# Optimization experiments

Measured on AMD Instinct MI355X. Metric: run time of the kernel, lower is better.

Reference implementation:

```python
import jax, jax.numpy as jnp
import numpy as np

SMOOTH = 1e-3
N_BASES = 256


def _bases():
    # bases[i, k] = k-th bit (LSB-first) of i, matching f'{i:08b}'[::-1]
    i = np.arange(N_BASES)[:, None]
    k = np.arange(8)[None, :]
    return jnp.asarray(((i >> k) & 1).astype(np.float32))  # [256, 8]


def _unfold(x):
    # x: [B, 2, Y, X] -> [B, 8, (Y+1)*(X+1)], matching F.unfold(kernel=(2,2), padding=1)
    B, C, Y, X = x.shape
    p = jnp.pad(x, ((0, 0), (0, 0), (1, 1), (1, 1)))
    cols = [p[:, c, ky:ky + Y + 1, kx:kx + X + 1]
            for c in range(2) for ky in range(2) for kx in range(2)]
    return jnp.stack(cols, axis=1).reshape(B, 8, (Y + 1) * (X + 1))


def _pair(pred_s, labels, raw, area, bases):
    # pred_s/labels/raw: [B, 2, Y, X]
    up = _unfold(pred_s)                       # [B, 8, L] sigmoid probs
    ul = _unfold(labels)                       # [B, 8, L] float 0/1
    ur = _unfold(raw)                          # [B, 8, L] logits
    uli = ul.astype(jnp.int32)
    B, _, L = up.shape

    # 8-bit neighbour code per point
    label_byte = sum(uli[:, k, :] << k for k in range(8))  # [B, L] int32

    # pred weight of the basis matching each point's label code (gather form of the masked loop)
    sel = bases[label_byte]                    # [B, L, 8]
    w_lab = 1.0 - jnp.linalg.norm(up.transpose(0, 2, 1) - sel, axis=-1) / 16.0  # [B, L]

    # sequential 256-way byte update, faithful to the original python loop
    up_sg = jax.lax.stop_gradient(up)
    d2 = ((up_sg ** 2).sum(1)[:, None, :]
          - 2.0 * jnp.einsum('bkl,nk->bnl', up_sg, bases)
          + (bases ** 2).sum(1)[None, :, None])              # [B, 256, L]
    w_all = 1.0 - jnp.sqrt(jnp.maximum(d2, 0.0)) / 16.0      # [B, 256, L]

    def body(i, byte):
        w = w_all[:, i, :]
        return jnp.where(w > byte.astype(w.dtype), jnp.full_like(byte, 0) + i, byte)

    pred_byte = jax.lax.fori_loop(0, N_BASES, body, jnp.zeros((B, L), jnp.int32))

    pred_areas = area[pred_byte]               # [B, L]
    label_areas = area[label_byte]             # [B, L]
    num = 2.0 * (w_lab * label_areas).sum(1)   # [B]
    denom = label_areas.sum(1) + pred_areas.sum(1)

    # per-batch BCE-with-logits on points whose label cube is empty or full
    mask = ((label_byte == 0) | (label_byte == 255)).astype(up.dtype)  # [B, L]
    x, y = ur, ul
    bce = jnp.maximum(x, 0.0) - x * y + jnp.log1p(jnp.exp(-jnp.abs(x)))  # [B, 8, L]
    vol = (bce * mask[:, None, :]).sum((1, 2)) / (8.0 * mask.sum(1))     # [B]
    return num, denom, vol


def _forward(pred, labels, area):
    pred_s = jax.nn.sigmoid(pred)
    bases = _bases()
    # overlapping z-pairs: [B, Z-1, 2, Y, X] -> vmap over pair axis
    ps = jnp.stack((pred_s[:, :-1], pred_s[:, 1:]), axis=2)
    ls = jnp.stack((labels[:, :-1], labels[:, 1:]), axis=2)
    rs = jnp.stack((pred[:, :-1], pred[:, 1:]), axis=2)
    num, denom, vol = jax.vmap(lambda a, b, c: _pair(a, b, c, area, bases),
                               in_axes=1)(ps, ls, rs)
    num, denom, vol = num.sum(0), denom.sum(0), vol.sum(0)  # [B]
    dice = 1.0 - (num + SMOOTH) / (denom + SMOOTH)
    return dice.mean() + vol.mean()


def setup_inputs() -> dict:
    key = jax.random.key(0)
    k1, k2, k3 = jax.random.split(key, 3)
    pred = jax.random.normal(k1, (2, 12, 192, 192), dtype=jnp.float32)
    labels = jax.random.bernoulli(k2, 0.5, (2, 12, 192, 192)).astype(jnp.float32)
    area = jax.random.uniform(k3, (256,), dtype=jnp.float32) * 2.0
    return {"pred": pred, "labels": labels, "area": area}


def reference(pred, labels, area):
    return _forward(pred, labels, area)
```

## Files before the change

### kernel.cpp

```cpp
#include <hip/hip_runtime.h>
#include <math.h>

#define NYX 192
#define NNODE 193
#define L_NODES (NNODE*NNODE)
#define NPAIR 11
#define NB 2
#define NCH 12
#define NZ 3
#define NGRP (NZ*NB)
#define NBLK 49
#define RECF 12
#define LN2f 0.69314718055994530942f


__global__ __launch_bounds__(256) void sdice_node(const float* __restrict__ pred,
                                                  const float* __restrict__ labels,
                                                  const float* __restrict__ area,
                                                  float* __restrict__ partials)
{
    const int z    = blockIdx.z;
    const int b    = blockIdx.y;
    const int lane = threadIdx.x & 63;
    const int wrow = threadIdx.x >> 6;
    const int j    = blockIdx.x * 4 + wrow;
    const int t    = lane;
    const int np   = (z == 2) ? 3 : 4;
    const int nch  = np + 1;
    const int c0   = z * 4;

    __shared__ float areas[256];
    __shared__ float sred[4][10];
    areas[threadIdx.x] = area[threadIdx.x];
    __syncthreads();

    float numA = 0.f, denA = 0.f;
    float bceA[4] = {0.f, 0.f, 0.f, 0.f};
    float cntA[4] = {0.f, 0.f, 0.f, 0.f};

    const bool act = (j < NNODE) && (t < 48);

    if (act) {
        const int  y0 = (j >= 1) ? (j - 1) : 0;
        const int  y1 = (j <= NYX - 1) ? j : (NYX - 1);
        const int  xo = t * 4;

        float    sigP[2][6], bcvP[2][6], sigC[2][6], bcvC[2][6];
        unsigned w5P[2], w5C[2];

        for (int cc = 0; cc < nch; ++cc) {
            const int ch = c0 + cc;
            const size_t base = (size_t)(b * NCH + ch) * (NYX * NYX);

            #pragma unroll
            for (int r = 0; r < 2; ++r) {
                const int  yy = r ? y1 : y0;
                const bool mm = r ? (j <= NYX - 1) : (j >= 1);
                const float4 p4 = *reinterpret_cast<const float4*>(pred   + base + (size_t)yy * NYX + xo);
                const float4 l4 = *reinterpret_cast<const float4*>(labels + base + (size_t)yy * NYX + xo);
                const float pe[4] = {p4.x, p4.y, p4.z, p4.w};
                const float le[4] = {l4.x, l4.y, l4.z, l4.w};
                unsigned bits = 0;
                #pragma unroll
                for (int e = 0; e < 4; ++e) {
                    const float pv = mm ? pe[e] : 0.f;
                    const float lv = mm ? le[e] : 0.f;
                    bits |= ((unsigned)lv) << e;
                    const float s = __builtin_amdgcn_rcpf(1.f + __expf(-pv));
                    sigC[r][e + 1] = mm ? s : 0.f;
                    bcvC[r][e + 1] = fmaxf(pv, 0.f) - pv * lv + __logf(1.f + __expf(-fabsf(pv)));
                }
                w5C[r] = bits << 1;
                sigC[r][5] = 0.f;
                bcvC[r][5] = LN2f;

                const float    sw = __shfl_up(sigC[r][4], 1);
                const float    bw = __shfl_up(bcvC[r][4], 1);
                const unsigned ww = (unsigned)__shfl_up((int)w5C[r], 1);
                sigC[r][0] = (t == 0) ? 0.f  : sw;
                bcvC[r][0] = (t == 0) ? LN2f : bw;
                w5C[r]    |= (t == 0) ? 0u   : ((ww >> 4) & 1u);
            }

            if (cc > 0) {
                const int pp = cc - 1;
                float pnum = 0.f, pden = 0.f, pbce = 0.f, pcnt = 0.f;
                #pragma unroll
                for (int i = 0; i < 5; ++i) {
                    if (i < 4 || t == 47) {
                        const unsigned b0 = (w5P[0] >> i) & 1u, b1 = (w5P[0] >> (i + 1)) & 1u;
                        const unsigned b2 = (w5P[1] >> i) & 1u, b3 = (w5P[1] >> (i + 1)) & 1u;
                        const unsigned b4 = (w5C[0] >> i) & 1u, b5 = (w5C[0] >> (i + 1)) & 1u;
                        const unsigned b6 = (w5C[1] >> i) & 1u, b7 = (w5C[1] >> (i + 1)) & 1u;
                        const unsigned byte = b0 | (b1 << 1) | (b2 << 2) | (b3 << 3)
                                            | (b4 << 4) | (b5 << 5) | (b6 << 6) | (b7 << 7);
                        float d2 = 0.f;
                        {
                            const float e0 = sigP[0][i]     - (float)b0;
                            const float e1 = sigP[0][i + 1] - (float)b1;
                            const float e2 = sigP[1][i]     - (float)b2;
                            const float e3 = sigP[1][i + 1] - (float)b3;
                            const float e4 = sigC[0][i]     - (float)b4;
                            const float e5 = sigC[0][i + 1] - (float)b5;
                            const float e6 = sigC[1][i]     - (float)b6;
                            const float e7 = sigC[1][i + 1] - (float)b7;
                            d2 = ((e0*e0 + e1*e1) + (e2*e2 + e3*e3)) + ((e4*e4 + e5*e5) + (e6*e6 + e7*e7));
                        }
                        const float w  = 1.f - sqrtf(d2) * (1.f / 16.f);
                        const float la = areas[byte];
                        pnum += w * la;
                        pden += la;
                        const bool msk = (byte == 0u) || (byte == 255u);
                        if (msk) {
                            pcnt += 1.f;
                            pbce += ((bcvP[0][i] + bcvP[0][i+1]) + (bcvP[1][i] + bcvP[1][i+1]))
                                  + ((bcvC[0][i] + bcvC[0][i+1]) + (bcvC[1][i] + bcvC[1][i+1]));
                        }
                    }
                }
                numA += pnum; denA += pden;
                bceA[pp] += pbce; cntA[pp] += pcnt;
            }

            #pragma unroll
            for (int r = 0; r < 2; ++r) {
                w5P[r] = w5C[r];
                #pragma unroll
                for (int q = 0; q < 6; ++q) { sigP[r][q] = sigC[r][q]; bcvP[r][q] = bcvC[r][q]; }
            }
        }
    }


    float v[10] = {numA, denA, bceA[0], bceA[1], bceA[2], bceA[3], cntA[0], cntA[1], cntA[2], cntA[3]};
    #pragma unroll
    for (int off = 32; off > 0; off >>= 1) {
        #pragma unroll
        for (int q = 0; q < 10; ++q) v[q] += __shfl_down(v[q], off);
    }
    if (lane == 0) {
        #pragma unroll
        for (int q = 0; q < 10; ++q) sred[wrow][q] = v[q];
    }
    __syncthreads();
    if (threadIdx.x == 0) {
        float s[10];
        #pragma unroll
        for (int q = 0; q < 10; ++q)
            s[q] = ((sred[0][q] + sred[1][q]) + (sred[2][q] + sred[3][q]));
        float* rec = partials + (size_t)((z * NB + b) * NBLK + blockIdx.x) * RECF;
        #pragma unroll
        for (int q = 0; q < 10; ++q) rec[q] = s[q];
        rec[10] = 0.f; rec[11] = 0.f;
    }
}

__global__ __launch_bounds__(384) void sdice_final(const float* __restrict__ partials,
                                                   const float* __restrict__ area,
                                                   float* __restrict__ out)
{
    __shared__ float gs[NGRP][10];
    const int g    = threadIdx.x >> 6;
    const int lane = threadIdx.x & 63;

    float v[10];
    #pragma unroll
    for (int q = 0; q < 10; ++q) v[q] = 0.f;
    if (lane < NBLK) {
        const float* rec = partials + (size_t)(g * NBLK + lane) * RECF;
        #pragma unroll
        for (int q = 0; q < 10; ++q) v[q] = rec[q];
    }
    #pragma unroll
    for (int off = 32; off > 0; off >>= 1) {
        #pragma unroll
        for (int q = 0; q < 10; ++q) v[q] += __shfl_down(v[q], off);
    }
    if (lane == 0) {
        #pragma unroll
        for (int q = 0; q < 10; ++q) gs[g][q] = v[q];
    }
    __syncthreads();

    if (threadIdx.x == 0) {
        const float a1 = area[1];
        float dice_sum = 0.f, vol_sum = 0.f;
        for (int b = 0; b < NB; ++b) {
            float numb = 0.f, denb = 0.f, volb = 0.f;
            for (int z = 0; z < NZ; ++z) {
                const int g2 = z * NB + b;
                const int np = (z == 2) ? 3 : 4;
                numb += 2.0f * gs[g2][0];
                denb += gs[g2][1];
                for (int pp = 0; pp < np; ++pp)
                    volb += gs[g2][2 + pp] / (8.0f * gs[g2][6 + pp]);
            }
            denb += (float)NPAIR * (float)L_NODES * a1;
            dice_sum += 1.0f - (numb + 0.001f) / (denb + 0.001f);
            vol_sum  += volb;
        }
        out[0] = dice_sum / (float)NB + vol_sum / (float)NB;
    }
}

extern "C" void kernel_launch(void* const* d_in, const int* in_sizes, int n_in,
                              void* d_out, int out_size, void* d_ws, size_t ws_size,
                              hipStream_t stream) {
    const float* pred   = (const float*)d_in[0];
    const float* labels = (const float*)d_in[1];
    const float* area   = (const float*)d_in[2];
    float* out  = (float*)d_out;
    float* part = (float*)d_ws;

    dim3 grid(NBLK, NB, NZ);
    sdice_node<<<grid, dim3(256), 0, stream>>>(pred, labels, area, part);
    sdice_final<<<1, 384, 0, stream>>>(part, area, out);
}
```

Measured before the change: 19.23 us.

## Fuse final reduction into node kernel via atomics and last-block ticket

```diff
diff --git a/kernel.cpp b/kernel.cpp
--- a/kernel.cpp
+++ b/kernel.cpp
@@ -10,14 +10,19 @@
 #define NZ 3
 #define NGRP (NZ*NB)
 #define NBLK 49
-#define RECF 12
+#define NBUCK 4
+#define TOTAL_BLOCKS (NBLK*NB*NZ)
 #define LN2f 0.69314718055994530942f
 
-
-__global__ __launch_bounds__(256) void sdice_node(const float* __restrict__ pred,
-                                                  const float* __restrict__ labels,
-                                                  const float* __restrict__ area,
-                                                  float* __restrict__ partials)
+#define ACC_LINES (NGRP*NBUCK)
+#define TICKET_OFF (ACC_LINES*16*sizeof(float))
+
+__global__ __launch_bounds__(256) void sdice_fused(const float* __restrict__ pred,
+                                                   const float* __restrict__ labels,
+                                                   const float* __restrict__ area,
+                                                   float* __restrict__ acc,
+                                                   unsigned* __restrict__ ticket,
+                                                   float* __restrict__ out)
 {
     const int z    = blockIdx.z;
     const int b    = blockIdx.y;
@@ -31,6 +36,9 @@
 
     __shared__ float areas[256];
     __shared__ float sred[4][10];
+    __shared__ float abuf[NGRP][NBUCK][10];
+    __shared__ float gs[NGRP][10];
+    __shared__ int   lastFlag;
     areas[threadIdx.x] = area[threadIdx.x];
     __syncthreads();
 
@@ -131,7 +139,6 @@
         }
     }
 
-
     float v[10] = {numA, denA, bceA[0], bceA[1], bceA[2], bceA[3], cntA[0], cntA[1], cntA[2], cntA[3]};
     #pragma unroll
     for (int off = 32; off > 0; off >>= 1) {
@@ -143,63 +150,55 @@
         for (int q = 0; q < 10; ++q) sred[wrow][q] = v[q];
     }
     __syncthreads();
+
     if (threadIdx.x == 0) {
         float s[10];
         #pragma unroll
         for (int q = 0; q < 10; ++q)
             s[q] = ((sred[0][q] + sred[1][q]) + (sred[2][q] + sred[3][q]));
-        float* rec = partials + (size_t)((z * NB + b) * NBLK + blockIdx.x) * RECF;
-        #pragma unroll
-        for (int q = 0; q < 10; ++q) rec[q] = s[q];
-        rec[10] = 0.f; rec[11] = 0.f;
-    }
-}
-
-__global__ __launch_bounds__(384) void sdice_final(const float* __restrict__ partials,
-                                                   const float* __restrict__ area,
-                                                   float* __restrict__ out)
-{
-    __shared__ float gs[NGRP][10];
-    const int g    = threadIdx.x >> 6;
-    const int lane = threadIdx.x & 63;
-
-    float v[10];
-    #pragma unroll
-    for (int q = 0; q < 10; ++q) v[q] = 0.f;
-    if (lane < NBLK) {
-        const float* rec = partials + (size_t)(g * NBLK + lane) * RECF;
-        #pragma unroll
-        for (int q = 0; q < 10; ++q) v[q] = rec[q];
-    }
-    #pragma unroll
-    for (int off = 32; off > 0; off >>= 1) {
-        #pragma unroll
-        for (int q = 0; q < 10; ++q) v[q] += __shfl_down(v[q], off);
-    }
-    if (lane == 0) {
-        #pragma unroll
-        for (int q = 0; q < 10; ++q) gs[g][q] = v[q];
+        float* gp = acc + (size_t)((z * NB + b) * NBUCK + (blockIdx.x & (NBUCK - 1))) * 16;
+        #pragma unroll
+        for (int q = 0; q < 10; ++q) atomicAdd(gp + q, s[q]);
+        asm volatile("s_waitcnt vmcnt(0)" ::: "memory");
+        const unsigned tk = atomicAdd(ticket, 1u);
+        lastFlag = (tk == TOTAL_BLOCKS - 1);
     }
     __syncthreads();
 
-    if (threadIdx.x == 0) {
-        const float a1 = area[1];
-        float dice_sum = 0.f, vol_sum = 0.f;
-        for (int b = 0; b < NB; ++b) {
-            float numb = 0.f, denb = 0.f, volb = 0.f;
-            for (int z = 0; z < NZ; ++z) {
-                const int g2 = z * NB + b;
-                const int np = (z == 2) ? 3 : 4;
-                numb += 2.0f * gs[g2][0];
-                denb += gs[g2][1];
-                for (int pp = 0; pp < np; ++pp)
-                    volb += gs[g2][2 + pp] / (8.0f * gs[g2][6 + pp]);
-            }
-            denb += (float)NPAIR * (float)L_NODES * a1;
-            dice_sum += 1.0f - (numb + 0.001f) / (denb + 0.001f);
-            vol_sum  += volb;
-        }
-        out[0] = dice_sum / (float)NB + vol_sum / (float)NB;
+    if (lastFlag) {
+        if (threadIdx.x < NGRP * NBUCK * 10) {
+            const int g  = threadIdx.x / (NBUCK * 10);
+            const int r  = threadIdx.x % (NBUCK * 10);
+            const int bu = r / 10;
+            const int q  = r % 10;
+            abuf[g][bu][q] = atomicAdd(acc + (size_t)(g * NBUCK + bu) * 16 + q, 0.0f);
+        }
+        __syncthreads();
+        if (threadIdx.x < NGRP * 10) {
+            const int g = threadIdx.x / 10;
+            const int q = threadIdx.x % 10;
+            gs[g][q] = ((abuf[g][0][q] + abuf[g][1][q]) + (abuf[g][2][q] + abuf[g][3][q]));
+        }
+        __syncthreads();
+        if (threadIdx.x == 0) {
+            const float a1 = areas[1];
+            float dice_sum = 0.f, vol_sum = 0.f;
+            for (int bb = 0; bb < NB; ++bb) {
+                float numb = 0.f, denb = 0.f, volb = 0.f;
+                for (int zz = 0; zz < NZ; ++zz) {
+                    const int g2 = zz * NB + bb;
+                    const int npz = (zz == 2) ? 3 : 4;
+                    numb += 2.0f * gs[g2][0];
+                    denb += gs[g2][1];
+                    for (int pp = 0; pp < npz; ++pp)
+                        volb += gs[g2][2 + pp] / (8.0f * gs[g2][6 + pp]);
+                }
+                denb += (float)NPAIR * (float)L_NODES * a1;
+                dice_sum += 1.0f - (numb + 0.001f) / (denb + 0.001f);
+                vol_sum  += volb;
+            }
+            out[0] = dice_sum / (float)NB + vol_sum / (float)NB;
+        }
     }
 }
 
@@ -209,10 +208,14 @@
     const float* pred   = (const float*)d_in[0];
     const float* labels = (const float*)d_in[1];
     const float* area   = (const float*)d_in[2];
-    float* out  = (float*)d_out;
-    float* part = (float*)d_ws;
+    float* out = (float*)d_out;
+    char*  ws  = (char*)d_ws;
+
+    float*    acc    = (float*)ws;
+    unsigned* ticket = (unsigned*)(ws + TICKET_OFF);
+
+    hipMemsetAsync(ws, 0, TICKET_OFF + sizeof(unsigned), stream);
 
     dim3 grid(NBLK, NB, NZ);
-    sdice_node<<<grid, dim3(256), 0, stream>>>(pred, labels, area, part);
-    sdice_final<<<1, 384, 0, stream>>>(part, area, out);
+    sdice_fused<<<grid, dim3(256), 0, stream>>>(pred, labels, area, acc, ticket, out);
 }
```

New measurement: 28.39 us. 47.6% more time.

## Fuse node and final kernels via cooperative grid sync, six rows per block

Applied to the files above, without the earlier changes.

```diff
diff --git a/kernel.cpp b/kernel.cpp
--- a/kernel.cpp
+++ b/kernel.cpp
@@ -1,5 +1,8 @@
 #include <hip/hip_runtime.h>
+#include <hip/hip_cooperative_groups.h>
 #include <math.h>
+
+namespace cg = cooperative_groups;
 
 #define NYX 192
 #define NNODE 193
@@ -9,31 +12,28 @@
 #define NCH 12
 #define NZ 3
 #define NGRP (NZ*NB)
-#define NBLK 49
+#define RPB 6
+#define NBLKX 33
 #define RECF 12
 #define LN2f 0.69314718055994530942f
 
 
-__global__ __launch_bounds__(256) void sdice_node(const float* __restrict__ pred,
-                                                  const float* __restrict__ labels,
-                                                  const float* __restrict__ area,
-                                                  float* __restrict__ partials)
+__device__ __forceinline__ void sdice_compute(const float* __restrict__ pred,
+                                              const float* __restrict__ labels,
+                                              float* __restrict__ rec,
+                                              const float areas[256],
+                                              float sred[RPB][10])
 {
     const int z    = blockIdx.z;
     const int b    = blockIdx.y;
     const int lane = threadIdx.x & 63;
     const int wrow = threadIdx.x >> 6;
-    const int j    = blockIdx.x * 4 + wrow;
+    const int j    = blockIdx.x * RPB + wrow;
     const int t    = lane;
     const int np   = (z == 2) ? 3 : 4;
     const int nch  = np + 1;
     const int c0   = z * 4;
 
-    __shared__ float areas[256];
-    __shared__ float sred[4][10];
-    areas[threadIdx.x] = area[threadIdx.x];
-    __syncthreads();
-
     float numA = 0.f, denA = 0.f;
     float bceA[4] = {0.f, 0.f, 0.f, 0.f};
     float cntA[4] = {0.f, 0.f, 0.f, 0.f};
@@ -41,9 +41,9 @@
     const bool act = (j < NNODE) && (t < 48);
 
     if (act) {
-        const int  y0 = (j >= 1) ? (j - 1) : 0;
-        const int  y1 = (j <= NYX - 1) ? j : (NYX - 1);
-        const int  xo = t * 4;
+        const int y0 = (j >= 1) ? (j - 1) : 0;
+        const int y1 = (j <= NYX - 1) ? j : (NYX - 1);
+        const int xo = t * 4;
 
         float    sigP[2][6], bcvP[2][6], sigC[2][6], bcvC[2][6];
         unsigned w5P[2], w5C[2];
@@ -94,18 +94,16 @@
                         const unsigned b6 = (w5C[1] >> i) & 1u, b7 = (w5C[1] >> (i + 1)) & 1u;
                         const unsigned byte = b0 | (b1 << 1) | (b2 << 2) | (b3 << 3)
                                             | (b4 << 4) | (b5 << 5) | (b6 << 6) | (b7 << 7);
-                        float d2 = 0.f;
-                        {
-                            const float e0 = sigP[0][i]     - (float)b0;
-                            const float e1 = sigP[0][i + 1] - (float)b1;
-                            const float e2 = sigP[1][i]     - (float)b2;
-                            const float e3 = sigP[1][i + 1] - (float)b3;
-                            const float e4 = sigC[0][i]     - (float)b4;
-                            const float e5 = sigC[0][i + 1] - (float)b5;
-                            const float e6 = sigC[1][i]     - (float)b6;
-                            const float e7 = sigC[1][i + 1] - (float)b7;
-                            d2 = ((e0*e0 + e1*e1) + (e2*e2 + e3*e3)) + ((e4*e4 + e5*e5) + (e6*e6 + e7*e7));
-                        }
+                        const float e0 = sigP[0][i]     - (float)b0;
+                        const float e1 = sigP[0][i + 1] - (float)b1;
+                        const float e2 = sigP[1][i]     - (float)b2;
+                        const float e3 = sigP[1][i + 1] - (float)b3;
+                        const float e4 = sigC[0][i]     - (float)b4;
+                        const float e5 = sigC[0][i + 1] - (float)b5;
+                        const float e6 = sigC[1][i]     - (float)b6;
+                        const float e7 = sigC[1][i + 1] - (float)b7;
+                        const float d2 = ((e0*e0 + e1*e1) + (e2*e2 + e3*e3))
+                                       + ((e4*e4 + e5*e5) + (e6*e6 + e7*e7));
                         const float w  = 1.f - sqrtf(d2) * (1.f / 16.f);
                         const float la = areas[byte];
                         pnum += w * la;
@@ -131,7 +129,6 @@
         }
     }
 
-
     float v[10] = {numA, denA, bceA[0], bceA[1], bceA[2], bceA[3], cntA[0], cntA[1], cntA[2], cntA[3]};
     #pragma unroll
     for (int off = 32; off > 0; off >>= 1) {
@@ -147,29 +144,31 @@
         float s[10];
         #pragma unroll
         for (int q = 0; q < 10; ++q)
-            s[q] = ((sred[0][q] + sred[1][q]) + (sred[2][q] + sred[3][q]));
-        float* rec = partials + (size_t)((z * NB + b) * NBLK + blockIdx.x) * RECF;
-        #pragma unroll
-        for (int q = 0; q < 10; ++q) rec[q] = s[q];
-        rec[10] = 0.f; rec[11] = 0.f;
-    }
-}
-
-__global__ __launch_bounds__(384) void sdice_final(const float* __restrict__ partials,
-                                                   const float* __restrict__ area,
-                                                   float* __restrict__ out)
-{
-    __shared__ float gs[NGRP][10];
-    const int g    = threadIdx.x >> 6;
+            s[q] = ((sred[0][q] + sred[1][q]) + (sred[2][q] + sred[3][q])) + (sred[4][q] + sred[5][q]);
+        float* rp = rec + (size_t)((z * NB + b) * NBLKX + blockIdx.x) * RECF;
+        #pragma unroll
+        for (int q = 0; q < 10; ++q) atomicExch(rp + q, s[q]);
+        asm volatile("s_waitcnt vmcnt(0)" ::: "memory");
+    }
+}
+
+__device__ __forceinline__ void sdice_finish(const float* __restrict__ rec,
+                                             const float* __restrict__ area,
+                                             float* __restrict__ out,
+                                             float gsb[NGRP][10])
+{
+    const int wrow = threadIdx.x >> 6;
     const int lane = threadIdx.x & 63;
 
     float v[10];
     #pragma unroll
     for (int q = 0; q < 10; ++q) v[q] = 0.f;
-    if (lane < NBLK) {
-        const float* rec = partials + (size_t)(g * NBLK + lane) * RECF;
-        #pragma unroll
-        for (int q = 0; q < 10; ++q) v[q] = rec[q];
+    if (lane < NBLKX) {
+        const float4* r4 = reinterpret_cast<const float4*>(rec + (size_t)(wrow * NBLKX + lane) * RECF);
+        const float4 a = r4[0], bb = r4[1], c = r4[2];
+        v[0]=a.x; v[1]=a.y; v[2]=a.z; v[3]=a.w;
+        v[4]=bb.x; v[5]=bb.y; v[6]=bb.z; v[7]=bb.w;
+        v[8]=c.x; v[9]=c.y;
     }
     #pragma unroll
     for (int off = 32; off > 0; off >>= 1) {
@@ -178,22 +177,21 @@
     }
     if (lane == 0) {
         #pragma unroll
-        for (int q = 0; q < 10; ++q) gs[g][q] = v[q];
-    }
-    __syncthreads();
-
+        for (int q = 0; q < 10; ++q) gsb[wrow][q] = v[q];
+    }
+    __syncthreads();
     if (threadIdx.x == 0) {
         const float a1 = area[1];
         float dice_sum = 0.f, vol_sum = 0.f;
-        for (int b = 0; b < NB; ++b) {
+        for (int bb = 0; bb < NB; ++bb) {
             float numb = 0.f, denb = 0.f, volb = 0.f;
-            for (int z = 0; z < NZ; ++z) {
-                const int g2 = z * NB + b;
-                const int np = (z == 2) ? 3 : 4;
-                numb += 2.0f * gs[g2][0];
-                denb += gs[g2][1];
-                for (int pp = 0; pp < np; ++pp)
-                    volb += gs[g2][2 + pp] / (8.0f * gs[g2][6 + pp]);
+            for (int zz = 0; zz < NZ; ++zz) {
+                const int g2 = zz * NB + bb;
+                const int npz = (zz == 2) ? 3 : 4;
+                numb += 2.0f * gsb[g2][0];
+                denb += gsb[g2][1];
+                for (int pp = 0; pp < npz; ++pp)
+                    volb += gsb[g2][2 + pp] / (8.0f * gsb[g2][6 + pp]);
             }
             denb += (float)NPAIR * (float)L_NODES * a1;
             dice_sum += 1.0f - (numb + 0.001f) / (denb + 0.001f);
@@ -201,6 +199,47 @@
         }
         out[0] = dice_sum / (float)NB + vol_sum / (float)NB;
     }
+}
+
+__global__ __launch_bounds__(384) void sdice_coop(const float* __restrict__ pred,
+                                                  const float* __restrict__ labels,
+                                                  const float* __restrict__ area,
+                                                  float* __restrict__ rec,
+                                                  float* __restrict__ out)
+{
+    __shared__ float areas[256];
+    __shared__ float sred[RPB][10];
+    __shared__ float gsb[NGRP][10];
+    if (threadIdx.x < 256) areas[threadIdx.x] = area[threadIdx.x];
+    __syncthreads();
+
+    sdice_compute(pred, labels, rec, areas, sred);
+
+    cg::this_grid().sync();
+
+    if (blockIdx.x == 0 && blockIdx.y == 0 && blockIdx.z == 0)
+        sdice_finish(rec, area, out, gsb);
+}
+
+
+__global__ __launch_bounds__(384) void sdice_node_fb(const float* __restrict__ pred,
+                                                     const float* __restrict__ labels,
+                                                     const float* __restrict__ area,
+                                                     float* __restrict__ rec)
+{
+    __shared__ float areas[256];
+    __shared__ float sred[RPB][10];
+    if (threadIdx.x < 256) areas[threadIdx.x] = area[threadIdx.x];
+    __syncthreads();
+    sdice_compute(pred, labels, rec, areas, sred);
+}
+
+__global__ __launch_bounds__(384) void sdice_final_fb(const float* __restrict__ rec,
+                                                      const float* __restrict__ area,
+                                                      float* __restrict__ out)
+{
+    __shared__ float gsb[NGRP][10];
+    sdice_finish(rec, area, out, gsb);
 }
 
 extern "C" void kernel_launch(void* const* d_in, const int* in_sizes, int n_in,
@@ -209,10 +248,15 @@
     const float* pred   = (const float*)d_in[0];
     const float* labels = (const float*)d_in[1];
     const float* area   = (const float*)d_in[2];
-    float* out  = (float*)d_out;
-    float* part = (float*)d_ws;
-
-    dim3 grid(NBLK, NB, NZ);
-    sdice_node<<<grid, dim3(256), 0, stream>>>(pred, labels, area, part);
-    sdice_final<<<1, 384, 0, stream>>>(part, area, out);
-}
+    float* out = (float*)d_out;
+    float* rec = (float*)d_ws;
+
+    dim3 grid(NBLKX, NB, NZ), blk(384, 1, 1);
+    void* args[5] = {(void*)&pred, (void*)&labels, (void*)&area, (void*)&rec, (void*)&out};
+    const hipError_t e = hipLaunchCooperativeKernel((void*)sdice_coop, grid, blk,
+                                                    args, 0u, stream);
+    if (e != hipSuccess) {
+        sdice_node_fb<<<grid, blk, 0, stream>>>(pred, labels, area, rec);
+        sdice_final_fb<<<1, blk, 0, stream>>>(rec, area, out);
+    }
+}
```

After: 54.86 us. 185% more time.
